# Kernel optimization log

Measured on AMD Instinct MI355X. Metric: run time of the kernel, lower is better.

Reference implementation:

```python
import jax, jax.numpy as jnp
import numpy as np

E = 512      # embedding / hidden size
L = 4        # num LSTM layers
B = 32       # batch
SE = 48      # encoder max len
SD = 48      # decoder max len
EV = 16000   # encoder vocab (emb1 has EV+1 rows)
DV = 16000   # decoder vocab (emb2 has DV+1 rows, lin3 outputs DV)


def _cell(x, h, c, Wih, Whh, bih, bhh):
    # single LSTM cell step, PyTorch gate order i,f,g,o
    g = x @ Wih.T + h @ Whh.T + bih + bhh
    i, f, gg, o = jnp.split(g, 4, axis=-1)
    c = jax.nn.sigmoid(f) * c + jax.nn.sigmoid(i) * jnp.tanh(gg)
    h = jax.nn.sigmoid(o) * jnp.tanh(c)
    return h, c


def _stack_cell(x, h, c, Wih, Whh, bih, bhh):
    # h, c: [L, B, E]; params stacked over layers [L, 4E, E] / [L, 4E]
    hs, cs = [], []
    inp = x
    for l in range(L):
        hn, cn = _cell(inp, h[l], c[l], Wih[l], Whh[l], bih[l], bhh[l])
        hs.append(hn); cs.append(cn)
        inp = hn
    return jnp.stack(hs), jnp.stack(cs)


def setup_inputs() -> dict:
    key = jax.random.key(0)
    ks = jax.random.split(key, 24)
    s = 0.02
    e_tokens = jax.random.randint(ks[0], (B, SE), 0, EV + 1, dtype=jnp.int32)
    e_lengths = jnp.sort(jax.random.randint(ks[1], (B,), 1, SE + 1, dtype=jnp.int32))[::-1]
    d_tokens = jax.random.randint(ks[2], (B, SD), 0, DV + 1, dtype=jnp.int32)
    emb1_w = jax.random.normal(ks[3], (EV + 1, E), jnp.float32) * s
    emb2_w = jax.random.normal(ks[4], (DV + 1, E), jnp.float32) * s
    emb2_w = emb2_w.at[0].set(0.0)  # padding_idx=0
    Wih1 = jax.random.normal(ks[5], (L, 4 * E, E), jnp.float32) * s
    Whh1 = jax.random.normal(ks[6], (L, 4 * E, E), jnp.float32) * s
    bih1 = jax.random.normal(ks[7], (L, 4 * E), jnp.float32) * s
    bhh1 = jax.random.normal(ks[8], (L, 4 * E), jnp.float32) * s
    W1 = jax.random.normal(ks[9], (SE, SE), jnp.float32) * s
    b1 = jax.random.normal(ks[10], (SE,), jnp.float32) * s
    W2 = jax.random.normal(ks[11], (E, SE + E), jnp.float32) * s
    b2 = jax.random.normal(ks[12], (E,), jnp.float32) * s
    Wih2 = jax.random.normal(ks[13], (L, 4 * E, E), jnp.float32) * s
    Whh2 = jax.random.normal(ks[14], (L, 4 * E, E), jnp.float32) * s
    bih2 = jax.random.normal(ks[15], (L, 4 * E), jnp.float32) * s
    bhh2 = jax.random.normal(ks[16], (L, 4 * E), jnp.float32) * s
    W3 = jax.random.normal(ks[17], (DV, E), jnp.float32) * s
    b3 = jax.random.normal(ks[18], (DV,), jnp.float32) * s
    return dict(e_tokens=e_tokens, e_lengths=e_lengths, d_tokens=d_tokens,
                emb1_w=emb1_w, emb2_w=emb2_w,
                Wih1=Wih1, Whh1=Whh1, bih1=bih1, bhh1=bhh1,
                W1=W1, b1=b1, W2=W2, b2=b2,
                Wih2=Wih2, Whh2=Whh2, bih2=bih2, bhh2=bhh2,
                W3=W3, b3=b3)


def reference(e_tokens, e_lengths, d_tokens, emb1_w, emb2_w,
              Wih1, Whh1, bih1, bhh1, W1, b1, W2, b2,
              Wih2, Whh2, bih2, bhh2, W3, b3):
    # ---- encoder: 4-layer LSTM over packed (length-masked) sequence ----
    ex = emb1_w[e_tokens]                      # [B, SE, E]
    h0 = jnp.zeros((L, B, E), ex.dtype)
    c0 = jnp.zeros((L, B, E), ex.dtype)

    def enc_step(carry, xt):
        h, c = carry
        x_t, t = xt
        nh, nc = _stack_cell(x_t, h, c, Wih1, Whh1, bih1, bhh1)
        m = (t < e_lengths)[:, None]           # [B,1]; freeze state past length (packed semantics)
        h = jnp.where(m, nh, h)
        c = jnp.where(m, nc, c)
        out = jnp.where(m, nh[-1], 0.0)        # pad_packed zeros beyond length
        return (h, c), out

    (h, c), outs = jax.lax.scan(enc_step, (h0, c0),
                                (ex.transpose(1, 0, 2), jnp.arange(SE)))
    upo = outs.transpose(1, 0, 2)              # [B, SE, E]
    upo_sum = upo.sum(axis=2)                  # [B, SE]; for the (faithful) context reduction

    dx = d_tokens[:, :-1].T                    # [SD-1, B] decoder inputs
    dy = d_tokens[:, 1:].T                     # [SD-1, B] labels

    def dec_step(carry, dl):
        h, c = carry
        d_t, l_t = dl
        # attention scores: dot(last_hid_top, upo) over embedding dim
        att = jnp.einsum('be,bse->bs', h[-1], upo)          # [B, SE]
        att = jax.nn.softmax(att @ W1.T + b1, axis=1)
        # faithful to original: (att[:,:,None]*upo).sum(dim=2) == att * upo.sum(-1)
        ctx = att * upo_sum                                  # [B, SE]
        de = emb2_w[d_t]                                     # [B, E]
        de = jnp.concatenate([ctx, de], axis=1) @ W2.T + b2  # [B, E]
        h, c = _stack_cell(de, h, c, Wih2, Whh2, bih2, bhh2)
        logits = h[-1] @ W3.T + b3                           # [B, DV]
        mask = (l_t != 0)
        lab = jnp.maximum(l_t - 1, 0)
        logp = jax.nn.log_softmax(logits, axis=-1)
        ce = -jnp.take_along_axis(logp, lab[:, None], axis=1)[:, 0]
        cnt = mask.sum()
        step_loss = jnp.where(cnt > 0,
                              jnp.where(mask, ce, 0.0).sum() / jnp.maximum(cnt, 1).astype(ce.dtype),
                              0.0)
        return (h, c), step_loss

    (_, _), losses = jax.lax.scan(dec_step, (h, c), (dx, dy))
    return losses.sum()
```

## Files before the change

### kernel.cpp

```cpp
#include <hip/hip_runtime.h>

#define EDIM 512
#define NL 4
#define NB 32
#define SEQ 48
#define SDD 48
#define DVV 16000
#define NBLK 128
#define NTHR 1024
#define NTILES (DVV/16)

#define BAR_OFF 0
#define WCE_OFF 256
#define H3F_OFF 512
#define HBF_OFF (H3F_OFF + NB*EDIM*4)
#define ZERO_BYTES (HBF_OFF + 2*NL*NB*EDIM*2)
#define DEB_OFF ZERO_BYTES
#define CWS_OFF (DEB_OFF + NB*EDIM*2)
#define UPO_OFF (CWS_OFF + (size_t)NL*NB*EDIM*4)
#define EXB_OFF (UPO_OFF + (size_t)NB*SEQ*EDIM*2)
#define CEP_OFF (EXB_OFF + (size_t)NB*SEQ*EDIM*2)
#define WI1_OFF (CEP_OFF + (size_t)NB*NTILES*4*4)
#define WH1_OFF (WI1_OFF + (size_t)NL*4*EDIM*EDIM*2)
#define WI2_OFF (WH1_OFF + (size_t)NL*4*EDIM*EDIM*2)
#define WH2_OFF (WI2_OFF + (size_t)NL*4*EDIM*EDIM*2)
#define W3B_OFF (WH2_OFF + (size_t)NL*4*EDIM*EDIM*2)
#define W2T_OFF (W3B_OFF + (size_t)DVV*EDIM*2)
#define BS1_OFF (W2T_OFF + (size_t)560*EDIM*2)
#define BS2_OFF (BS1_OFF + (size_t)NL*4*EDIM*4)

typedef __bf16 bf16x8 __attribute__((ext_vector_type(8)));
typedef float floatx4 __attribute__((ext_vector_type(4)));
typedef unsigned int uint4e __attribute__((ext_vector_type(4)));
typedef unsigned short ushort4e __attribute__((ext_vector_type(4)));

struct Params {
  const int *etok, *elen, *dtok;
  const float *emb2;
  const float *W1, *b1, *b2;
  const float *b3;
  float* out;
  char* ws;
};

__device__ __forceinline__ float wred_sum(float v) {
#pragma unroll
  for (int i = 32; i > 0; i >>= 1) v += __shfl_xor(v, i, 64);
  return v;
}
__device__ __forceinline__ float wred_max(float v) {
#pragma unroll
  for (int i = 32; i > 0; i >>= 1) v = fmaxf(v, __shfl_xor(v, i, 64));
  return v;
}
__device__ __forceinline__ float sigm(float x) { return 1.f / (1.f + __expf(-x)); }
__device__ __forceinline__ float tanh_f(float x) { return 1.f - 2.f / (__expf(2.f * x) + 1.f); }
__device__ __forceinline__ unsigned short f2bf(float f) {
  unsigned int u = __float_as_uint(f);
  return (unsigned short)((u + 0x7fffu + ((u >> 16) & 1u)) >> 16);
}
__device__ __forceinline__ float bf2f(unsigned short u) {
  return __uint_as_float(((unsigned int)u) << 16);
}
__device__ __forceinline__ bf16x8 ld_bf8(const unsigned short* p) {
  return __builtin_bit_cast(bf16x8, *(const uint4e*)p);
}
__device__ __forceinline__ floatx4 mfma16(bf16x8 a, bf16x8 b, floatx4 c) {
  return __builtin_amdgcn_mfma_f32_16x16x32_bf16(a, b, c, 0, 0, 0);
}

__device__ __forceinline__ void gsync(int* bar, int ph) {
  __syncthreads();
  if (threadIdx.x == 0) {
    __hip_atomic_fetch_add(&bar[0], 1, __ATOMIC_RELEASE, __HIP_MEMORY_SCOPE_AGENT);
    const int target = ph * NBLK;
    while (__hip_atomic_load(&bar[0], __ATOMIC_RELAXED, __HIP_MEMORY_SCOPE_AGENT) < target)
      __builtin_amdgcn_s_sleep(16);
    (void)__hip_atomic_load(&bar[0], __ATOMIC_ACQUIRE, __HIP_MEMORY_SCOPE_AGENT);
  }
  __syncthreads();
}

__device__ void gemm4g(const unsigned short* Wi, const unsigned short* Wh,
                       const unsigned short* xsrc, int xstr, const unsigned short* hsrc,
                       int et, int tid, float* parts) {
  const int wid = tid >> 6, lane = tid & 63, ln = lane & 15, kq = lane >> 4;
  const int g = wid & 3, ks = wid >> 2;
  const size_t n = (size_t)g * 512 + et * 16 + ln;
  const bool isH = (ks >= 2);
  const unsigned short* wr = (isH ? Wh : Wi) + n * EDIM;
  const unsigned short* ap = isH ? hsrc : xsrc;
  const int as = isH ? EDIM : xstr;
  const unsigned short* a0b = ap + (size_t)ln * as;
  const unsigned short* a1b = ap + (size_t)(16 + ln) * as;
  const int k0 = (ks & 1) * 256 + kq * 8;
  floatx4 acc0 = {0.f, 0.f, 0.f, 0.f}, acc1 = {0.f, 0.f, 0.f, 0.f};
#pragma unroll
  for (int c8 = 0; c8 < 8; ++c8) {
    const int kk = k0 + c8 * 32;
    bf16x8 bf = ld_bf8(wr + kk);
    bf16x8 a0 = ld_bf8(a0b + kk);
    bf16x8 a1 = ld_bf8(a1b + kk);
    acc0 = mfma16(a0, bf, acc0);
    acc1 = mfma16(a1, bf, acc1);
  }
  const int base = ((ks * 4 + g) * 2) * 256 + lane;
#pragma unroll
  for (int r = 0; r < 4; ++r) {
    parts[base + r * 64] = acc0[r];
    parts[base + 256 + r * 64] = acc1[r];
  }
}

__device__ void gate_combine(const float* parts, float* gates,
                             const float* bsum, int et, int tid) {
  for (int v = tid; v < 2048; v += NTHR) {
    const int ln = v & 15, b = (v >> 4) & 31, g = v >> 9;
    const int mt = b >> 4, kq = (b >> 2) & 3, r = b & 3;
    const int lane = kq * 16 + ln;
    float s = 0.f;
#pragma unroll
    for (int ks = 0; ks < 4; ++ks)
      s += parts[((ks * 4 + g) * 2 + mt) * 256 + r * 64 + lane];
    gates[v] = s + bsum[g * 512 + et * 16 + ln];
  }
}

__global__ __launch_bounds__(NTHR) void seq2seq_kernel(Params p) {
  __shared__ float sm_parts[8192];
  __shared__ float sm_gates[2048];
  __shared__ float sm_c[2048];
  __shared__ float sm_attn[768];
  const int tid = threadIdx.x, blk = blockIdx.x;
  char* wsb = p.ws;
  int* bar = (int*)wsb;
  float* wce = (float*)(wsb + WCE_OFF);
  float* h3f = (float*)(wsb + H3F_OFF);
  unsigned short* hbf = (unsigned short*)(wsb + HBF_OFF);
  unsigned short* deb = (unsigned short*)(wsb + DEB_OFF);
  float* cws = (float*)(wsb + CWS_OFF);
  unsigned short* upo = (unsigned short*)(wsb + UPO_OFF);
  unsigned short* exb = (unsigned short*)(wsb + EXB_OFF);
  float* cep = (float*)(wsb + CEP_OFF);
  const unsigned short* wi1 = (const unsigned short*)(wsb + WI1_OFF);
  const unsigned short* wh1 = (const unsigned short*)(wsb + WH1_OFF);
  const unsigned short* wi2 = (const unsigned short*)(wsb + WI2_OFF);
  const unsigned short* wh2 = (const unsigned short*)(wsb + WH2_OFF);
  const unsigned short* w3b = (const unsigned short*)(wsb + W3B_OFF);
  const unsigned short* w2t = (const unsigned short*)(wsb + W2T_OFF);
  const float* bs1 = (const float*)(wsb + BS1_OFF);
  const float* bs2 = (const float*)(wsb + BS2_OFF);
  int ph = 0;
  float total_loss = 0.f;

  {
    const int li = blk >> 5, et = blk & 31;
    sm_c[tid] = 0.f; sm_c[tid + 1024] = 0.f;
    int mylen = 0;
    if (tid < 512) mylen = p.elen[tid >> 4];
    __syncthreads();
    for (int d = 0; d < SEQ + NL - 1; ++d) {
      const int t = d - li;
      if (t >= 0 && t < SEQ) {
        const int tp = t & 1, tq = tp ^ 1;
        const unsigned short* xsrc; int xstr;
        if (li == 0) { xsrc = exb + (size_t)t * EDIM; xstr = SEQ * EDIM; }
        else { xsrc = hbf + ((size_t)tp * NL + (li - 1)) * NB * EDIM; xstr = EDIM; }
        const unsigned short* hsrc = hbf + ((size_t)tq * NL + li) * NB * EDIM;
        gemm4g(wi1 + (size_t)li * 2048 * EDIM, wh1 + (size_t)li * 2048 * EDIM,
               xsrc, xstr, hsrc, et, tid, sm_parts);
        __syncthreads();
        gate_combine(sm_parts, sm_gates, bs1 + li * 2048, et, tid);
        __syncthreads();
        if (tid < 512) {
          const int b = tid >> 4, ln = tid & 15, e = et * 16 + ln;
          const bool act = t < mylen;
          const size_t hup = ((size_t)tp * NL + li) * NB * EDIM + (size_t)b * EDIM + e;
          const size_t hdn = ((size_t)tq * NL + li) * NB * EDIM + (size_t)b * EDIM + e;
          unsigned short hnew;
          if (act) {
            const float ig = sigm(sm_gates[tid]);
            const float fg = sigm(sm_gates[512 + tid]);
            const float gg = tanh_f(sm_gates[1024 + tid]);
            const float og = sigm(sm_gates[1536 + tid]);
            const float cn = fg * sm_c[tid] + ig * gg;
            sm_c[tid] = cn;
            const float h = og * tanh_f(cn);
            hnew = f2bf(h);
            if (li == 3) h3f[b * EDIM + e] = h;
          } else {
            hnew = hbf[hdn];
          }
          hbf[hup] = hnew;
          if (li == 3) upo[((size_t)b * SEQ + t) * EDIM + e] = act ? hnew : (unsigned short)0;
        }
        if (t == SEQ - 1) {
          __syncthreads();
          if (tid < 512) {
            const int b = tid >> 4, ln = tid & 15;
            cws[((size_t)li * NB + b) * EDIM + et * 16 + ln] = sm_c[tid];
          }
        }
      }
      gsync(bar, ++ph);
    }
  }

  for (int t = 0; t < SDD - 1; ++t) {
    const int pw = t & 1, pr = pw ^ 1;
    if (blk < NB) {
      const int b = blk;
      const int wid = tid >> 6, lane = tid & 63;
      const float* h3r = h3f + b * EDIM + lane * 8;
      float hq[8];
      const float4 h4a = *(const float4*)h3r;
      const float4 h4b = *(const float4*)(h3r + 4);
      hq[0]=h4a.x; hq[1]=h4a.y; hq[2]=h4a.z; hq[3]=h4a.w;
      hq[4]=h4b.x; hq[5]=h4b.y; hq[6]=h4b.z; hq[7]=h4b.w;
      const int tok = p.dtok[b * SDD + t];
      if (tid < EDIM) sm_attn[240 + tid] = p.emb2[(size_t)tok * EDIM + tid];
      for (int s = wid; s < SEQ; s += 16) {
        const unsigned short* up = upo + ((size_t)b * SEQ + s) * EDIM + lane * 8;
        const uint4e uv = *(const uint4e*)up;
        float dv = 0.f, sv = 0.f;
#pragma unroll
        for (int j = 0; j < 4; ++j) {
          const unsigned int w = uv[j];
          const float lo = __uint_as_float(w << 16);
          const float hi = __uint_as_float(w & 0xffff0000u);
          dv = fmaf(lo, hq[2 * j], dv); sv += lo;
          dv = fmaf(hi, hq[2 * j + 1], dv); sv += hi;
        }
        dv = wred_sum(dv); sv = wred_sum(sv);
        if (lane == 0) { sm_attn[s] = dv; sm_attn[64 + s] = sv; }
      }
      if (t == 0 && tid >= 512) {
#pragma unroll
        for (int j = 0; j < 4; ++j) {
          const int v = (tid - 512) * 4 + j;
          const int l = v >> 9, rem = v & 511, b2 = rem >> 4, ln = rem & 15;
          sm_c[v] = cws[((size_t)l * NB + b2) * EDIM + blk * 16 + ln];
        }
      }
      if (t >= 2 && blk == 0 && wid == 8) {
        float v = (lane < NB) ? wce[lane] : 0.f;
        v = wred_sum(v);
        if (lane == 0) total_loss += v;
      }
      __syncthreads();
      if (wid == 0) {
        float y = -1e30f;
        if (lane < SEQ) {
          y = p.b1[lane];
          const float* w1r = p.W1 + lane * SEQ;
          for (int s = 0; s < SEQ; ++s) y = fmaf(sm_attn[s], w1r[s], y);
        }
        const float m = wred_max(y);
        const float ex = (lane < SEQ) ? __expf(y - m) : 0.f;
        const float S = wred_sum(ex);
        if (lane < SEQ) sm_attn[192 + lane] = (ex / S) * sm_attn[64 + lane];
      }
      __syncthreads();
      {
        const int q = tid >> 8, tn = tid & 255, e2 = tn * 2;
        const int kb = q * 140;
        float a0 = (q == 0) ? p.b2[e2] : 0.f;
        float a1 = (q == 0) ? p.b2[e2 + 1] : 0.f;
        for (int k = kb; k < kb + 140; ++k) {
          const float av = sm_attn[192 + k];
          const unsigned int w = *(const unsigned int*)(w2t + (size_t)k * 512 + e2);
          a0 = fmaf(av, __uint_as_float(w << 16), a0);
          a1 = fmaf(av, __uint_as_float(w & 0xffff0000u), a1);
        }
        sm_parts[q * 512 + e2] = a0;
        sm_parts[q * 512 + e2 + 1] = a1;
      }
      __syncthreads();
      if (tid < 512) {
        const float s = sm_parts[tid] + sm_parts[512 + tid] + sm_parts[1024 + tid] + sm_parts[1536 + tid];
        deb[b * EDIM + tid] = f2bf(s);
      }
    } else if (t >= 1) {
      const int idx = (blk - 32) * 16 + (tid >> 6);
      if (idx < NTILES) {
        const int lane = tid & 63, ln = lane & 15, kq = lane >> 4;
        const unsigned short* wrow = w3b + ((size_t)idx * 16 + ln) * EDIM + kq * 8;
        const unsigned short* arow = hbf + ((size_t)pr * NL + 3) * NB * EDIM;
        const unsigned short* a0p = arow + (size_t)ln * EDIM + kq * 8;
        const unsigned short* a1p = a0p + 16 * EDIM;
        floatx4 acc0 = {0.f,0.f,0.f,0.f}, acc1 = {0.f,0.f,0.f,0.f};
#pragma unroll
        for (int c = 0; c < 16; ++c) {
          bf16x8 bf = ld_bf8(wrow + c * 32);
          bf16x8 a0 = ld_bf8(a0p + c * 32);
          bf16x8 a1 = ld_bf8(a1p + c * 32);
          acc0 = mfma16(a0, bf, acc0);
          acc1 = mfma16(a1, bf, acc1);
        }
        const float bv = p.b3[idx * 16 + ln];
        const int v = idx * 16 + ln;
        const int step = t - 1;
#pragma unroll
        for (int mt = 0; mt < 2; ++mt) {
#pragma unroll
          for (int r = 0; r < 4; ++r) {
            const int b = mt * 16 + kq * 4 + r;
            const int ltok = p.dtok[b * SDD + step + 1];
            const int lab = (ltok > 0) ? ltok - 1 : 0;
            const float lv = (mt ? acc1[r] : acc0[r]) + bv;
            float m = lv, lb = (v == lab) ? lv : -1e30f;
#pragma unroll
            for (int st = 1; st < 16; st <<= 1) m = fmaxf(m, __shfl_xor(m, st, 64));
            float se = __expf(lv - m);
#pragma unroll
            for (int st = 1; st < 16; st <<= 1) se += __shfl_xor(se, st, 64);
#pragma unroll
            for (int st = 1; st < 16; st <<= 1) lb = fmaxf(lb, __shfl_xor(lb, st, 64));
            if (ln == 0) {
              float* cp = cep + ((size_t)b * NTILES + idx) * 4;
              cp[0] = m; cp[1] = se; cp[2] = lb;
            }
          }
        }
      }
    }
    gsync(bar, ++ph);
    for (int l = 0; l < NL; ++l) {
      if (blk < NB) {
        const unsigned short* xsrc = (l == 0) ? deb : hbf + ((size_t)pw * NL + (l - 1)) * NB * EDIM;
        const unsigned short* hsrc = hbf + ((size_t)pr * NL + l) * NB * EDIM;
        gemm4g(wi2 + (size_t)l * 2048 * EDIM, wh2 + (size_t)l * 2048 * EDIM,
               xsrc, EDIM, hsrc, blk, tid, sm_parts);
        __syncthreads();
        gate_combine(sm_parts, sm_gates, bs2 + l * 2048, blk, tid);
        __syncthreads();
        if (tid < 512) {
          const int b = tid >> 4, ln = tid & 15, e = blk * 16 + ln;
          const float ig = sigm(sm_gates[tid]);
          const float fg = sigm(sm_gates[512 + tid]);
          const float gg = tanh_f(sm_gates[1024 + tid]);
          const float og = sigm(sm_gates[1536 + tid]);
          const float cn = fg * sm_c[l * 512 + tid] + ig * gg;
          sm_c[l * 512 + tid] = cn;
          const float h = og * tanh_f(cn);
          hbf[((size_t)pw * NL + l) * NB * EDIM + (size_t)b * EDIM + e] = f2bf(h);
          if (l == 3) h3f[b * EDIM + e] = h;
        }
      } else if (l == 0 && blk >= 32 && blk < 64 && t >= 1) {
        const int b = blk - 32;
        float m = -1e30f, s = 0.f, lb = -1e30f;
        if (tid < NTILES) {
          const float* cp = cep + ((size_t)b * NTILES + tid) * 4;
          m = cp[0]; s = cp[1]; lb = cp[2];
        }
        const int wid = tid >> 6, lane = tid & 63;
        const float M = wred_max(m);
        float sc = s * __expf(m - M);
        sc = wred_sum(sc);
        const float wl = wred_max(lb);
        if (lane == 0) { sm_parts[wid] = M; sm_parts[16 + wid] = sc; sm_parts[32 + wid] = wl; }
        __syncthreads();
        if (tid == 0) {
          float M2 = -1e30f, LB = -1e30f;
          for (int w = 0; w < 16; ++w) M2 = fmaxf(M2, sm_parts[w]);
          float S = 0.f;
          for (int w = 0; w < 16; ++w) S += sm_parts[16 + w] * __expf(sm_parts[w] - M2);
          for (int w = 0; w < 16; ++w) LB = fmaxf(LB, sm_parts[32 + w]);
          const int step = t - 1;
          const int ltok = p.dtok[b * SDD + step + 1];
          int cnt = 0;
          for (int b2 = 0; b2 < NB; ++b2) cnt += (p.dtok[b2 * SDD + step + 1] != 0);
          wce[b] = (ltok != 0 && cnt > 0) ? (-(LB - M2 - __logf(S))) / (float)cnt : 0.f;
        }
      }
      gsync(bar, ++ph);
    }
  }

  {
    const int t46 = SDD - 2;
    if (blk >= 32) {
      const int idx = (blk - 32) * 16 + (tid >> 6);
      if (idx < NTILES) {
        const int lane = tid & 63, ln = lane & 15, kq = lane >> 4;
        const unsigned short* wrow = w3b + ((size_t)idx * 16 + ln) * EDIM + kq * 8;
        const unsigned short* arow = hbf + ((size_t)0 * NL + 3) * NB * EDIM;
        const unsigned short* a0p = arow + (size_t)ln * EDIM + kq * 8;
        const unsigned short* a1p = a0p + 16 * EDIM;
        floatx4 acc0 = {0.f,0.f,0.f,0.f}, acc1 = {0.f,0.f,0.f,0.f};
#pragma unroll
        for (int c = 0; c < 16; ++c) {
          bf16x8 bf = ld_bf8(wrow + c * 32);
          bf16x8 a0 = ld_bf8(a0p + c * 32);
          bf16x8 a1 = ld_bf8(a1p + c * 32);
          acc0 = mfma16(a0, bf, acc0);
          acc1 = mfma16(a1, bf, acc1);
        }
        const float bv = p.b3[idx * 16 + ln];
        const int v = idx * 16 + ln;
#pragma unroll
        for (int mt = 0; mt < 2; ++mt) {
#pragma unroll
          for (int r = 0; r < 4; ++r) {
            const int b = mt * 16 + kq * 4 + r;
            const int ltok = p.dtok[b * SDD + t46 + 1];
            const int lab = (ltok > 0) ? ltok - 1 : 0;
            const float lv = (mt ? acc1[r] : acc0[r]) + bv;
            float m = lv, lb = (v == lab) ? lv : -1e30f;
#pragma unroll
            for (int st = 1; st < 16; st <<= 1) m = fmaxf(m, __shfl_xor(m, st, 64));
            float se = __expf(lv - m);
#pragma unroll
            for (int st = 1; st < 16; st <<= 1) se += __shfl_xor(se, st, 64);
#pragma unroll
            for (int st = 1; st < 16; st <<= 1) lb = fmaxf(lb, __shfl_xor(lb, st, 64));
            if (ln == 0) {
              float* cp = cep + ((size_t)b * NTILES + idx) * 4;
              cp[0] = m; cp[1] = se; cp[2] = lb;
            }
          }
        }
      }
    } else if (blk == 0 && (tid >> 6) == 8) {
      float v = ((tid & 63) < NB) ? wce[tid & 63] : 0.f;
      v = wred_sum(v);
      if ((tid & 63) == 0) total_loss += v;
    }
    gsync(bar, ++ph);
    if (blk >= 32 && blk < 64) {
      const int b = blk - 32;
      float m = -1e30f, s = 0.f, lb = -1e30f;
      if (tid < NTILES) {
        const float* cp = cep + ((size_t)b * NTILES + tid) * 4;
        m = cp[0]; s = cp[1]; lb = cp[2];
      }
      const int wid = tid >> 6, lane = tid & 63;
      const float M = wred_max(m);
      float sc = s * __expf(m - M);
      sc = wred_sum(sc);
      const float wl = wred_max(lb);
      if (lane == 0) { sm_parts[wid] = M; sm_parts[16 + wid] = sc; sm_parts[32 + wid] = wl; }
      __syncthreads();
      if (tid == 0) {
        float M2 = -1e30f, LB = -1e30f;
        for (int w = 0; w < 16; ++w) M2 = fmaxf(M2, sm_parts[w]);
        float S = 0.f;
        for (int w = 0; w < 16; ++w) S += sm_parts[16 + w] * __expf(sm_parts[w] - M2);
        for (int w = 0; w < 16; ++w) LB = fmaxf(LB, sm_parts[32 + w]);
        const int ltok = p.dtok[b * SDD + t46 + 1];
        int cnt = 0;
        for (int b2 = 0; b2 < NB; ++b2) cnt += (p.dtok[b2 * SDD + t46 + 1] != 0);
        wce[b] = (ltok != 0 && cnt > 0) ? (-(LB - M2 - __logf(S))) / (float)cnt : 0.f;
      }
    }
    gsync(bar, ++ph);
    if (blk == 0 && (tid >> 6) == 8) {
      float v = ((tid & 63) < NB) ? wce[tid & 63] : 0.f;
      v = wred_sum(v);
      if ((tid & 63) == 0) { total_loss += v; p.out[0] = total_loss; }
    }
  }
}

__global__ __launch_bounds__(256) void convert_kernel(
    const float* Wih1, const float* Whh1, const float* Wih2, const float* Whh2,
    const float* W3, const float* emb1, const int* etok, const float* W2,
    const float* bih1, const float* bhh1, const float* bih2, const float* bhh2,
    char* wsb) {
  const long NW = (long)NL * 4 * EDIM * EDIM / 4;
  const long NW3 = (long)DVV * EDIM / 4;
  const long NEX = (long)NB * SEQ * EDIM / 4;
  const long NW2T = (long)560 * EDIM / 4;
  const long BF16_TOTAL = 4 * NW + NW3 + NEX + NW2T;
  const long NBS = (long)NL * 4 * EDIM / 4;
  const long total = BF16_TOTAL + 2 * NBS;
  for (long g = (long)blockIdx.x * blockDim.x + threadIdx.x; g < total;
       g += (long)gridDim.x * blockDim.x) {
    if (g >= BF16_TOTAL) {
      long off = g - BF16_TOTAL;
      const float *A, *Bp; float* D;
      if (off < NBS) { A = bih1; Bp = bhh1; D = (float*)(wsb + BS1_OFF); }
      else { off -= NBS; A = bih2; Bp = bhh2; D = (float*)(wsb + BS2_OFF); }
      float4 x = ((const float4*)A)[off];
      const float4 y = ((const float4*)Bp)[off];
      x.x += y.x; x.y += y.y; x.z += y.z; x.w += y.w;
      ((float4*)D)[off] = x;
      continue;
    }
    float4 v;
    unsigned short* dst;
    long off;
    if (g < 4 * NW) {
      const float* src;
      if (g < NW)           { src = Wih1; dst = (unsigned short*)(wsb + WI1_OFF); off = g; }
      else if (g < 2 * NW)  { src = Whh1; dst = (unsigned short*)(wsb + WH1_OFF); off = g - NW; }
      else if (g < 3 * NW)  { src = Wih2; dst = (unsigned short*)(wsb + WI2_OFF); off = g - 2 * NW; }
      else                  { src = Whh2; dst = (unsigned short*)(wsb + WH2_OFF); off = g - 3 * NW; }
      v = *((const float4*)src + off);
    } else if (g < 4 * NW + NW3) {
      off = g - 4 * NW;
      v = *((const float4*)W3 + off);
      dst = (unsigned short*)(wsb + W3B_OFF);
    } else if (g < 4 * NW + NW3 + NEX) {
      const long e4 = g - 4 * NW - NW3;
      const int k4 = (int)(e4 & 127);
      const long bt = e4 >> 7;
      const int tok = etok[bt];
      v = *((const float4*)(emb1 + (size_t)tok * EDIM) + k4);
      dst = (unsigned short*)(wsb + EXB_OFF);
      off = bt * 128 + k4;
    } else {
      off = g - 4 * NW - NW3 - NEX;
      const int e = (int)(off & 127) * 4;
      const int k = (int)(off >> 7);
      v.x = W2[(size_t)(e + 0) * (SEQ + EDIM) + k];
      v.y = W2[(size_t)(e + 1) * (SEQ + EDIM) + k];
      v.z = W2[(size_t)(e + 2) * (SEQ + EDIM) + k];
      v.w = W2[(size_t)(e + 3) * (SEQ + EDIM) + k];
      dst = (unsigned short*)(wsb + W2T_OFF);
    }
    ushort4e o;
    o.x = f2bf(v.x); o.y = f2bf(v.y); o.z = f2bf(v.z); o.w = f2bf(v.w);
    *(ushort4e*)(dst + off * 4) = o;
  }
}

extern "C" void kernel_launch(void* const* d_in, const int* in_sizes, int n_in,
                              void* d_out, int out_size, void* d_ws, size_t ws_size,
                              hipStream_t stream) {
  (void)in_sizes; (void)n_in; (void)out_size; (void)ws_size;
  const int* etok = (const int*)d_in[0];
  const int* elen = (const int*)d_in[1];
  const int* dtok = (const int*)d_in[2];
  const float* emb1 = (const float*)d_in[3];
  const float* emb2 = (const float*)d_in[4];
  const float* Wih1 = (const float*)d_in[5];
  const float* Whh1 = (const float*)d_in[6];
  const float* bih1 = (const float*)d_in[7];
  const float* bhh1 = (const float*)d_in[8];
  const float* W1 = (const float*)d_in[9];
  const float* b1 = (const float*)d_in[10];
  const float* W2 = (const float*)d_in[11];
  const float* b2 = (const float*)d_in[12];
  const float* Wih2 = (const float*)d_in[13];
  const float* Whh2 = (const float*)d_in[14];
  const float* bih2 = (const float*)d_in[15];
  const float* bhh2 = (const float*)d_in[16];
  const float* W3 = (const float*)d_in[17];
  const float* b3 = (const float*)d_in[18];

  hipMemsetAsync(d_ws, 0, ZERO_BYTES, stream);
  hipLaunchKernelGGL(convert_kernel, dim3(4096), dim3(256), 0, stream,
                     Wih1, Whh1, Wih2, Whh2, W3, emb1, etok, W2,
                     bih1, bhh1, bih2, bhh2, (char*)d_ws);

  Params prm;
  prm.etok = etok; prm.elen = elen; prm.dtok = dtok;
  prm.emb2 = emb2;
  prm.W1 = W1; prm.b1 = b1; prm.b2 = b2;
  prm.b3 = b3;
  prm.out = (float*)d_out;
  prm.ws = (char*)d_ws;
  void* args[] = { &prm };
  hipLaunchCooperativeKernel((const void*)seq2seq_kernel, dim3(NBLK), dim3(NTHR), args, 0, stream);
}
```

Baseline: 6.624 ms.

## Use cache-bypassing loads/stores for cross-block data and drop acquire in grid barrier

```diff
diff --git a/kernel.cpp b/kernel.cpp
--- a/kernel.cpp
+++ b/kernel.cpp
@@ -59,14 +59,55 @@
   unsigned int u = __float_as_uint(f);
   return (unsigned short)((u + 0x7fffu + ((u >> 16) & 1u)) >> 16);
 }
-__device__ __forceinline__ float bf2f(unsigned short u) {
-  return __uint_as_float(((unsigned int)u) << 16);
-}
 __device__ __forceinline__ bf16x8 ld_bf8(const unsigned short* p) {
   return __builtin_bit_cast(bf16x8, *(const uint4e*)p);
 }
 __device__ __forceinline__ floatx4 mfma16(bf16x8 a, bf16x8 b, floatx4 c) {
   return __builtin_amdgcn_mfma_f32_16x16x32_bf16(a, b, c, 0, 0, 0);
+}
+
+__device__ __forceinline__ uint4e ld_b128_llc(const void* p) {
+  uint4e v;
+  asm volatile("global_load_dwordx4 %0, %1, off sc0 sc1\n\ts_waitcnt vmcnt(0)"
+               : "=&v"(v) : "v"(p) : "memory");
+  return v;
+}
+__device__ __forceinline__ unsigned int ld_b32_llc(const void* p) {
+  unsigned int v;
+  asm volatile("global_load_dword %0, %1, off sc0 sc1\n\ts_waitcnt vmcnt(0)"
+               : "=&v"(v) : "v"(p) : "memory");
+  return v;
+}
+__device__ __forceinline__ unsigned short ld_b16_llc(const void* p) {
+  unsigned short v;
+  asm volatile("global_load_ushort %0, %1, off sc0 sc1\n\ts_waitcnt vmcnt(0)"
+               : "=&v"(v) : "v"(p) : "memory");
+  return v;
+}
+__device__ __forceinline__ void st_b32_llc(void* p, unsigned int v) {
+  asm volatile("global_store_dword %0, %1, off sc0 sc1" :: "v"(p), "v"(v) : "memory");
+}
+__device__ __forceinline__ void st_b16_llc(void* p, unsigned short v) {
+  asm volatile("global_store_short %0, %1, off sc0 sc1" :: "v"(p), "v"(v) : "memory");
+}
+__device__ __forceinline__ void st_b128_llc(void* p, uint4e v) {
+  asm volatile("global_store_dwordx4 %0, %1, off sc0 sc1" :: "v"(p), "v"(v) : "memory");
+}
+__device__ __forceinline__ void ld8_llc(const void* p0, const void* p1,
+                                        uint4e* o0, uint4e* o1) {
+  asm volatile(
+      "global_load_dwordx4 %0, %8, off sc0 sc1\n\t"
+      "global_load_dwordx4 %1, %8, off offset:64 sc0 sc1\n\t"
+      "global_load_dwordx4 %2, %8, off offset:128 sc0 sc1\n\t"
+      "global_load_dwordx4 %3, %8, off offset:192 sc0 sc1\n\t"
+      "global_load_dwordx4 %4, %9, off sc0 sc1\n\t"
+      "global_load_dwordx4 %5, %9, off offset:64 sc0 sc1\n\t"
+      "global_load_dwordx4 %6, %9, off offset:128 sc0 sc1\n\t"
+      "global_load_dwordx4 %7, %9, off offset:192 sc0 sc1\n\t"
+      "s_waitcnt vmcnt(0)"
+      : "=&v"(o0[0]), "=&v"(o0[1]), "=&v"(o0[2]), "=&v"(o0[3]),
+        "=&v"(o1[0]), "=&v"(o1[1]), "=&v"(o1[2]), "=&v"(o1[3])
+      : "v"(p0), "v"(p1) : "memory");
 }
 
 __device__ __forceinline__ void gsync(int* bar, int ph) {
@@ -75,8 +116,7 @@
     __hip_atomic_fetch_add(&bar[0], 1, __ATOMIC_RELEASE, __HIP_MEMORY_SCOPE_AGENT);
     const int target = ph * NBLK;
     while (__hip_atomic_load(&bar[0], __ATOMIC_RELAXED, __HIP_MEMORY_SCOPE_AGENT) < target)
-      __builtin_amdgcn_s_sleep(16);
-    (void)__hip_atomic_load(&bar[0], __ATOMIC_ACQUIRE, __HIP_MEMORY_SCOPE_AGENT);
+      __builtin_amdgcn_s_sleep(8);
   }
   __syncthreads();
 }
@@ -95,14 +135,23 @@
   const unsigned short* a1b = ap + (size_t)(16 + ln) * as;
   const int k0 = (ks & 1) * 256 + kq * 8;
   floatx4 acc0 = {0.f, 0.f, 0.f, 0.f}, acc1 = {0.f, 0.f, 0.f, 0.f};
-#pragma unroll
-  for (int c8 = 0; c8 < 8; ++c8) {
-    const int kk = k0 + c8 * 32;
-    bf16x8 bf = ld_bf8(wr + kk);
-    bf16x8 a0 = ld_bf8(a0b + kk);
-    bf16x8 a1 = ld_bf8(a1b + kk);
-    acc0 = mfma16(a0, bf, acc0);
-    acc1 = mfma16(a1, bf, acc1);
+  uint4e x0[4], x1[4];
+#pragma unroll
+  for (int h = 0; h < 2; ++h) {
+    const int kb = k0 + h * 128;
+    bf16x8 w0 = ld_bf8(wr + kb);
+    bf16x8 w1 = ld_bf8(wr + kb + 32);
+    bf16x8 w2 = ld_bf8(wr + kb + 64);
+    bf16x8 w3 = ld_bf8(wr + kb + 96);
+    ld8_llc(a0b + kb, a1b + kb, x0, x1);
+    acc0 = mfma16(__builtin_bit_cast(bf16x8, x0[0]), w0, acc0);
+    acc1 = mfma16(__builtin_bit_cast(bf16x8, x1[0]), w0, acc1);
+    acc0 = mfma16(__builtin_bit_cast(bf16x8, x0[1]), w1, acc0);
+    acc1 = mfma16(__builtin_bit_cast(bf16x8, x1[1]), w1, acc1);
+    acc0 = mfma16(__builtin_bit_cast(bf16x8, x0[2]), w2, acc0);
+    acc1 = mfma16(__builtin_bit_cast(bf16x8, x1[2]), w2, acc1);
+    acc0 = mfma16(__builtin_bit_cast(bf16x8, x0[3]), w3, acc0);
+    acc1 = mfma16(__builtin_bit_cast(bf16x8, x1[3]), w3, acc1);
   }
   const int base = ((ks * 4 + g) * 2) * 256 + lane;
 #pragma unroll
@@ -123,6 +172,60 @@
     for (int ks = 0; ks < 4; ++ks)
       s += parts[((ks * 4 + g) * 2 + mt) * 256 + r * 64 + lane];
     gates[v] = s + bsum[g * 512 + et * 16 + ln];
+  }
+}
+
+__device__ void logits_tile(const unsigned short* w3b, const unsigned short* hbase,
+                            const float* b3, const int* dtok, float* cep,
+                            int tile, int tid, int step) {
+  const int lane = tid & 63, ln = lane & 15, kq = lane >> 4;
+  const unsigned short* wrow = w3b + ((size_t)tile * 16 + ln) * EDIM + kq * 8;
+  const unsigned short* a0p = hbase + (size_t)ln * EDIM + kq * 8;
+  const unsigned short* a1p = a0p + 16 * EDIM;
+  floatx4 acc0 = {0.f, 0.f, 0.f, 0.f}, acc1 = {0.f, 0.f, 0.f, 0.f};
+  uint4e x0[4], x1[4];
+#pragma unroll
+  for (int h = 0; h < 4; ++h) {
+    const int kb = h * 128;
+    bf16x8 w0 = ld_bf8(wrow + kb);
+    bf16x8 w1 = ld_bf8(wrow + kb + 32);
+    bf16x8 w2 = ld_bf8(wrow + kb + 64);
+    bf16x8 w3 = ld_bf8(wrow + kb + 96);
+    ld8_llc(a0p + kb, a1p + kb, x0, x1);
+    acc0 = mfma16(__builtin_bit_cast(bf16x8, x0[0]), w0, acc0);
+    acc1 = mfma16(__builtin_bit_cast(bf16x8, x1[0]), w0, acc1);
+    acc0 = mfma16(__builtin_bit_cast(bf16x8, x0[1]), w1, acc0);
+    acc1 = mfma16(__builtin_bit_cast(bf16x8, x1[1]), w1, acc1);
+    acc0 = mfma16(__builtin_bit_cast(bf16x8, x0[2]), w2, acc0);
+    acc1 = mfma16(__builtin_bit_cast(bf16x8, x1[2]), w2, acc1);
+    acc0 = mfma16(__builtin_bit_cast(bf16x8, x0[3]), w3, acc0);
+    acc1 = mfma16(__builtin_bit_cast(bf16x8, x1[3]), w3, acc1);
+  }
+  const float bv = b3[tile * 16 + ln];
+  const int v = tile * 16 + ln;
+#pragma unroll
+  for (int mt = 0; mt < 2; ++mt) {
+#pragma unroll
+    for (int r = 0; r < 4; ++r) {
+      const int b = mt * 16 + kq * 4 + r;
+      const int ltok = dtok[b * SDD + step + 1];
+      const int lab = (ltok > 0) ? ltok - 1 : 0;
+      const float lv = (mt ? acc1[r] : acc0[r]) + bv;
+      float m = lv, lb = (v == lab) ? lv : -1e30f;
+#pragma unroll
+      for (int st = 1; st < 16; st <<= 1) m = fmaxf(m, __shfl_xor(m, st, 64));
+      float se = __expf(lv - m);
+#pragma unroll
+      for (int st = 1; st < 16; st <<= 1) se += __shfl_xor(se, st, 64);
+#pragma unroll
+      for (int st = 1; st < 16; st <<= 1) lb = fmaxf(lb, __shfl_xor(lb, st, 64));
+      if (ln == 0) {
+        uint4e pk;
+        pk.x = __float_as_uint(m); pk.y = __float_as_uint(se);
+        pk.z = __float_as_uint(lb); pk.w = 0u;
+        st_b128_llc(cep + ((size_t)b * NTILES + tile) * 4, pk);
+      }
+    }
   }
 }
 
@@ -187,18 +290,20 @@
             sm_c[tid] = cn;
             const float h = og * tanh_f(cn);
             hnew = f2bf(h);
-            if (li == 3) h3f[b * EDIM + e] = h;
+            if (li == 3) st_b32_llc(h3f + b * EDIM + e, __float_as_uint(h));
           } else {
-            hnew = hbf[hdn];
+            hnew = ld_b16_llc(hbf + hdn);
           }
-          hbf[hup] = hnew;
-          if (li == 3) upo[((size_t)b * SEQ + t) * EDIM + e] = act ? hnew : (unsigned short)0;
+          st_b16_llc(hbf + hup, hnew);
+          if (li == 3) st_b16_llc(upo + ((size_t)b * SEQ + t) * EDIM + e,
+                                  act ? hnew : (unsigned short)0);
         }
         if (t == SEQ - 1) {
           __syncthreads();
           if (tid < 512) {
             const int b = tid >> 4, ln = tid & 15;
-            cws[((size_t)li * NB + b) * EDIM + et * 16 + ln] = sm_c[tid];
+            st_b32_llc(cws + ((size_t)li * NB + b) * EDIM + et * 16 + ln,
+                       __float_as_uint(sm_c[tid]));
           }
         }
       }
@@ -213,10 +318,15 @@
       const int wid = tid >> 6, lane = tid & 63;
       const float* h3r = h3f + b * EDIM + lane * 8;
       float hq[8];
-      const float4 h4a = *(const float4*)h3r;
-      const float4 h4b = *(const float4*)(h3r + 4);
-      hq[0]=h4a.x; hq[1]=h4a.y; hq[2]=h4a.z; hq[3]=h4a.w;
-      hq[4]=h4b.x; hq[5]=h4b.y; hq[6]=h4b.z; hq[7]=h4b.w;
+      {
+        const uint4e va = ld_b128_llc(h3r);
+        const uint4e vb = ld_b128_llc(h3r + 4);
+#pragma unroll
+        for (int j = 0; j < 4; ++j) {
+          hq[j] = __uint_as_float(va[j]);
+          hq[4 + j] = __uint_as_float(vb[j]);
+        }
+      }
       const int tok = p.dtok[b * SDD + t];
       if (tid < EDIM) sm_attn[240 + tid] = p.emb2[(size_t)tok * EDIM + tid];
       for (int s = wid; s < SEQ; s += 16) {
@@ -243,7 +353,7 @@
         }
       }
       if (t >= 2 && blk == 0 && wid == 8) {
-        float v = (lane < NB) ? wce[lane] : 0.f;
+        float v = (lane < NB) ? __uint_as_float(ld_b32_llc(wce + lane)) : 0.f;
         v = wred_sum(v);
         if (lane == 0) total_loss += v;
       }
@@ -278,51 +388,13 @@
       __syncthreads();
       if (tid < 512) {
         const float s = sm_parts[tid] + sm_parts[512 + tid] + sm_parts[1024 + tid] + sm_parts[1536 + tid];
-        deb[b * EDIM + tid] = f2bf(s);
+        st_b16_llc(deb + b * EDIM + tid, f2bf(s));
       }
     } else if (t >= 1) {
-      const int idx = (blk - 32) * 16 + (tid >> 6);
-      if (idx < NTILES) {
-        const int lane = tid & 63, ln = lane & 15, kq = lane >> 4;
-        const unsigned short* wrow = w3b + ((size_t)idx * 16 + ln) * EDIM + kq * 8;
-        const unsigned short* arow = hbf + ((size_t)pr * NL + 3) * NB * EDIM;
-        const unsigned short* a0p = arow + (size_t)ln * EDIM + kq * 8;
-        const unsigned short* a1p = a0p + 16 * EDIM;
-        floatx4 acc0 = {0.f,0.f,0.f,0.f}, acc1 = {0.f,0.f,0.f,0.f};
-#pragma unroll
-        for (int c = 0; c < 16; ++c) {
-          bf16x8 bf = ld_bf8(wrow + c * 32);
-          bf16x8 a0 = ld_bf8(a0p + c * 32);
-          bf16x8 a1 = ld_bf8(a1p + c * 32);
-          acc0 = mfma16(a0, bf, acc0);
-          acc1 = mfma16(a1, bf, acc1);
-        }
-        const float bv = p.b3[idx * 16 + ln];
-        const int v = idx * 16 + ln;
-        const int step = t - 1;
-#pragma unroll
-        for (int mt = 0; mt < 2; ++mt) {
-#pragma unroll
-          for (int r = 0; r < 4; ++r) {
-            const int b = mt * 16 + kq * 4 + r;
-            const int ltok = p.dtok[b * SDD + step + 1];
-            const int lab = (ltok > 0) ? ltok - 1 : 0;
-            const float lv = (mt ? acc1[r] : acc0[r]) + bv;
-            float m = lv, lb = (v == lab) ? lv : -1e30f;
-#pragma unroll
-            for (int st = 1; st < 16; st <<= 1) m = fmaxf(m, __shfl_xor(m, st, 64));
-            float se = __expf(lv - m);
-#pragma unroll
-            for (int st = 1; st < 16; st <<= 1) se += __shfl_xor(se, st, 64);
-#pragma unroll
-            for (int st = 1; st < 16; st <<= 1) lb = fmaxf(lb, __shfl_xor(lb, st, 64));
-            if (ln == 0) {
-              float* cp = cep + ((size_t)b * NTILES + idx) * 4;
-              cp[0] = m; cp[1] = se; cp[2] = lb;
-            }
-          }
-        }
-      }
+      const int tile = (tid >> 6) * 96 + (blk - 32);
+      if (tile < NTILES)
+        logits_tile(w3b, hbf + ((size_t)pr * NL + 3) * NB * EDIM,
+                    p.b3, p.dtok, cep, tile, tid, t - 1);
     }
     gsync(bar, ++ph);
     for (int l = 0; l < NL; ++l) {
@@ -343,15 +415,15 @@
           const float cn = fg * sm_c[l * 512 + tid] + ig * gg;
           sm_c[l * 512 + tid] = cn;
           const float h = og * tanh_f(cn);
-          hbf[((size_t)pw * NL + l) * NB * EDIM + (size_t)b * EDIM + e] = f2bf(h);
-          if (l == 3) h3f[b * EDIM + e] = h;
+          st_b16_llc(hbf + ((size_t)pw * NL + l) * NB * EDIM + (size_t)b * EDIM + e, f2bf(h));
+          if (l == 3) st_b32_llc(h3f + b * EDIM + e, __float_as_uint(h));
         }
       } else if (l == 0 && blk >= 32 && blk < 64 && t >= 1) {
         const int b = blk - 32;
         float m = -1e30f, s = 0.f, lb = -1e30f;
         if (tid < NTILES) {
-          const float* cp = cep + ((size_t)b * NTILES + tid) * 4;
-          m = cp[0]; s = cp[1]; lb = cp[2];
+          const uint4e v = ld_b128_llc(cep + ((size_t)b * NTILES + tid) * 4);
+          m = __uint_as_float(v.x); s = __uint_as_float(v.y); lb = __uint_as_float(v.z);
         }
         const int wid = tid >> 6, lane = tid & 63;
         const float M = wred_max(m);
@@ -370,7 +442,8 @@
           const int ltok = p.dtok[b * SDD + step + 1];
           int cnt = 0;
           for (int b2 = 0; b2 < NB; ++b2) cnt += (p.dtok[b2 * SDD + step + 1] != 0);
-          wce[b] = (ltok != 0 && cnt > 0) ? (-(LB - M2 - __logf(S))) / (float)cnt : 0.f;
+          const float val = (ltok != 0 && cnt > 0) ? (-(LB - M2 - __logf(S))) / (float)cnt : 0.f;
+          st_b32_llc(wce + b, __float_as_uint(val));
         }
       }
       gsync(bar, ++ph);
@@ -380,49 +453,12 @@
   {
     const int t46 = SDD - 2;
     if (blk >= 32) {
-      const int idx = (blk - 32) * 16 + (tid >> 6);
-      if (idx < NTILES) {
-        const int lane = tid & 63, ln = lane & 15, kq = lane >> 4;
-        const unsigned short* wrow = w3b + ((size_t)idx * 16 + ln) * EDIM + kq * 8;
-        const unsigned short* arow = hbf + ((size_t)0 * NL + 3) * NB * EDIM;
-        const unsigned short* a0p = arow + (size_t)ln * EDIM + kq * 8;
-        const unsigned short* a1p = a0p + 16 * EDIM;
-        floatx4 acc0 = {0.f,0.f,0.f,0.f}, acc1 = {0.f,0.f,0.f,0.f};
-#pragma unroll
-        for (int c = 0; c < 16; ++c) {
-          bf16x8 bf = ld_bf8(wrow + c * 32);
-          bf16x8 a0 = ld_bf8(a0p + c * 32);
-          bf16x8 a1 = ld_bf8(a1p + c * 32);
-          acc0 = mfma16(a0, bf, acc0);
-          acc1 = mfma16(a1, bf, acc1);
-        }
-        const float bv = p.b3[idx * 16 + ln];
-        const int v = idx * 16 + ln;
-#pragma unroll
-        for (int mt = 0; mt < 2; ++mt) {
-#pragma unroll
-          for (int r = 0; r < 4; ++r) {
-            const int b = mt * 16 + kq * 4 + r;
-            const int ltok = p.dtok[b * SDD + t46 + 1];
-            const int lab = (ltok > 0) ? ltok - 1 : 0;
-            const float lv = (mt ? acc1[r] : acc0[r]) + bv;
-            float m = lv, lb = (v == lab) ? lv : -1e30f;
-#pragma unroll
-            for (int st = 1; st < 16; st <<= 1) m = fmaxf(m, __shfl_xor(m, st, 64));
-            float se = __expf(lv - m);
-#pragma unroll
-            for (int st = 1; st < 16; st <<= 1) se += __shfl_xor(se, st, 64);
-#pragma unroll
-            for (int st = 1; st < 16; st <<= 1) lb = fmaxf(lb, __shfl_xor(lb, st, 64));
-            if (ln == 0) {
-              float* cp = cep + ((size_t)b * NTILES + idx) * 4;
-              cp[0] = m; cp[1] = se; cp[2] = lb;
-            }
-          }
-        }
-      }
+      const int tile = (tid >> 6) * 96 + (blk - 32);
+      if (tile < NTILES)
+        logits_tile(w3b, hbf + ((size_t)0 * NL + 3) * NB * EDIM,
+                    p.b3, p.dtok, cep, tile, tid, t46);
     } else if (blk == 0 && (tid >> 6) == 8) {
-      float v = ((tid & 63) < NB) ? wce[tid & 63] : 0.f;
+      float v = ((tid & 63) < NB) ? __uint_as_float(ld_b32_llc(wce + (tid & 63))) : 0.f;
       v = wred_sum(v);
       if ((tid & 63) == 0) total_loss += v;
     }
@@ -431,8 +467,8 @@
       const int b = blk - 32;
       float m = -1e30f, s = 0.f, lb = -1e30f;
       if (tid < NTILES) {
-        const float* cp = cep + ((size_t)b * NTILES + tid) * 4;
-        m = cp[0]; s = cp[1]; lb = cp[2];
+        const uint4e v = ld_b128_llc(cep + ((size_t)b * NTILES + tid) * 4);
+        m = __uint_as_float(v.x); s = __uint_as_float(v.y); lb = __uint_as_float(v.z);
       }
       const int wid = tid >> 6, lane = tid & 63;
       const float M = wred_max(m);
@@ -450,12 +486,13 @@
         const int ltok = p.dtok[b * SDD + t46 + 1];
         int cnt = 0;
         for (int b2 = 0; b2 < NB; ++b2) cnt += (p.dtok[b2 * SDD + t46 + 1] != 0);
-        wce[b] = (ltok != 0 && cnt > 0) ? (-(LB - M2 - __logf(S))) / (float)cnt : 0.f;
+        const float val = (ltok != 0 && cnt > 0) ? (-(LB - M2 - __logf(S))) / (float)cnt : 0.f;
+        st_b32_llc(wce + b, __float_as_uint(val));
       }
     }
     gsync(bar, ++ph);
     if (blk == 0 && (tid >> 6) == 8) {
-      float v = ((tid & 63) < NB) ? wce[tid & 63] : 0.f;
+      float v = ((tid & 63) < NB) ? __uint_as_float(ld_b32_llc(wce + (tid & 63))) : 0.f;
       v = wred_sum(v);
       if ((tid & 63) == 0) { total_loss += v; p.out[0] = total_loss; }
     }
```

Result: no change. 6.624 ms (+0.0%).
